# Kernel optimization log

Measured on AMD Instinct MI355X. Metric: run time of the kernel, lower is better.

## Reference

```python
import jax, jax.numpy as jnp
import numpy as np

B, T = 16, 512
S = T - 16  # sequence length after three 5x5 VALID convs and pool (H: T-4-4-4-5+1)
H = 64      # GRU hidden size


def setup_inputs() -> dict:
    key = jax.random.key(0)
    ks = jax.random.split(key, 20)
    def prm(k, shape, s=0.02):
        return jax.random.normal(k, shape, dtype=jnp.float32) * s
    return {
        "evaluation": jax.random.normal(ks[0], (B, 128, T), dtype=jnp.float32),
        "template":   jax.random.normal(ks[1], (B, 128, T), dtype=jnp.float32),
        "conv1_w": prm(ks[2], (16, 1, 5, 5), 0.05),  "conv1_b": prm(ks[3], (16,)),
        "conv2_w": prm(ks[4], (32, 16, 5, 5), 0.05), "conv2_b": prm(ks[5], (32,)),
        "conv3_w": prm(ks[6], (64, 32, 5, 5), 0.05), "conv3_b": prm(ks[7], (64,)),
        "lin1_w": prm(ks[8], (64, 3712)), "lin1_b": prm(ks[9], (64,)),
        "W_ih": prm(ks[10], (192, 64), 0.1), "W_hh": prm(ks[11], (192, 64), 0.1),
        "b_ih": prm(ks[12], (192,)),          "b_hh": prm(ks[13], (192,)),
        "att_w": prm(ks[14], (1, 64)),  "att_b": prm(ks[15], (1,)),
        "lin3_w": prm(ks[16], (128, 64)), "lin3_b": prm(ks[17], (128,)),
        "cls_w": prm(ks[18], (2, 128)),   "cls_b": prm(ks[19], (2,)),
    }


def _conv(x, w, b):
    # x: (N, C, H, W), w: (O, C, kh, kw), VALID, stride 1
    y = jax.lax.conv_general_dilated(x, w, (1, 1), 'VALID',
                                     dimension_numbers=('NCHW', 'OIHW', 'NCHW'))
    return y + b[None, :, None, None]


def _gru_seq(x, W_ih, W_hh, b_ih, b_hh):
    # x: (L, 64). One hidden state carried over the whole length (this mirrors
    # the torch module threading h0/h1 across samples in its Python loop).
    gi = x @ W_ih.T + b_ih  # (L, 192) input gates precomputed
    def step(h, gi_t):
        gh = W_hh @ h + b_hh
        r = jax.nn.sigmoid(gi_t[:H] + gh[:H])
        z = jax.nn.sigmoid(gi_t[H:2 * H] + gh[H:2 * H])
        n = jnp.tanh(gi_t[2 * H:] + r * gh[2 * H:])
        h_new = (1.0 - z) * n + z * h
        return h_new, h_new
    _, hs = jax.lax.scan(step, jnp.zeros((H,), x.dtype), gi)
    return hs  # (L, 64)


def reference(evaluation, template, conv1_w, conv1_b, conv2_w, conv2_b,
              conv3_w, conv3_b, lin1_w, lin1_b, W_ih, W_hh, b_ih, b_hh,
              att_w, att_b, lin3_w, lin3_b, cls_w, cls_b):
    # Shared conv trunk on stacked eval+template batch
    x = jnp.concatenate([evaluation, template], axis=0)      # (2B, 128, T)
    x = jnp.transpose(x, (0, 2, 1))[:, None]                 # (2B, 1, T, 128)
    x = _conv(x, conv1_w, conv1_b)                           # (2B, 16, T-4, 124)
    x = _conv(x, conv2_w, conv2_b)                           # (2B, 32, T-8, 120)
    x = _conv(x, conv3_w, conv3_b)                           # (2B, 64, T-12, 116)
    x = jax.lax.reduce_window(x, -jnp.inf, jax.lax.max,
                              (1, 1, 5, 2), (1, 1, 1, 2), 'VALID')  # (2B, 64, S, 58)
    # torch does a raw per-sample reshape (64, S, 58) -> (S, 3712)
    x = x.reshape(2 * B, S, 3712)
    x = x @ lin1_w.T + lin1_b                                # (2B, S, 64)
    # GRU: hidden carried across the batch -> one long scan per branch
    E = _gru_seq(x[:B].reshape(B * S, H), W_ih, W_hh, b_ih, b_hh).reshape(B, S, H)
    Tm = _gru_seq(x[B:].reshape(B * S, H), W_ih, W_hh, b_ih, b_hh).reshape(B, S, H)
    # alignment_weights[m, n] = <E[m], Tm[n]>, softmax over m (dim=0 per sample)
    A = jax.nn.softmax(jnp.einsum('bmd,bnd->bmn', E, Tm), axis=1)
    Tp = jnp.einsum('bmn,bnd->bmd', A, Tm)                   # template_prim
    dist = jnp.abs(Tp - E)                                    # (B, S, 64)
    att = jax.nn.softmax(jnp.einsum('bsd,d->bs', E, att_w[0]) + att_b[0], axis=1)
    rep = jnp.einsum('bs,bsd->bd', att, dist)                 # (B, 64)
    h = jax.nn.relu(rep)
    h = jax.nn.relu(h @ lin3_w.T + lin3_b)
    return h @ cls_w.T + cls_b                                # (B, 2)
```

## Files before the change

### kernel.cpp

```cpp
#include <hip/hip_runtime.h>
#include <hip/hip_bf16.h>
#include <math.h>


#define DEVI static __device__ __forceinline__
typedef __attribute__((ext_vector_type(8))) short short8;
typedef __attribute__((ext_vector_type(4))) float f32x4;
typedef __attribute__((ext_vector_type(8))) float f32x8;
typedef unsigned short ushort_t;

DEVI float fsig(float x)   { return 1.f / (1.f + __expf(-x)); }
DEVI float ftanh_(float x) { return 2.f / (1.f + __expf(-2.f * x)) - 1.f; }
DEVI float bf2f(ushort_t u) { union { unsigned int i; float f; } v; v.i = ((unsigned int)u) << 16; return v.f; }
DEVI ushort_t f2bf(float f) {
    union { float f; unsigned int i; } v; v.f = f;
    unsigned int r = v.i + 0x7FFF + ((v.i >> 16) & 1);
    return (ushort_t)(r >> 16);
}
DEVI f32x8 bf2f8(short8 s) {
    f32x8 r;
#pragma unroll
    for (int k = 0; k < 8; k++) r[k] = bf2f((ushort_t)s[k]);
    return r;
}
DEVI f32x8 max8(f32x8 a, f32x8 b) {
    f32x8 r;
#pragma unroll
    for (int k = 0; k < 8; k++) r[k] = fmaxf(a[k], b[k]);
    return r;
}

DEVI void glds16(const ushort_t* g, ushort_t* l)
{
    __builtin_amdgcn_global_load_lds(
        (const __attribute__((address_space(1))) void*)g,
        (__attribute__((address_space(3))) void*)l, 16, 0, 0);
}

__global__ void pack_w2(const float* __restrict__ w2, ushort_t* __restrict__ w2p)
{
    for (int idx = blockIdx.x * 256 + threadIdx.x; idx < 15360; idx += gridDim.x * 256) {
        int kh = idx / 3072, rem = idx % 3072;
        int kw = rem / 512;
        int co = (rem >> 4) & 31, ci = rem & 15;
        float v = (kw < 5) ? w2[((co * 16 + ci) * 5 + kh) * 5 + kw] : 0.f;
        w2p[idx] = f2bf(v);
    }
}
__global__ void pack_w3(const float* __restrict__ w3, ushort_t* __restrict__ w3p)
{
    for (int idx = blockIdx.x * 256 + threadIdx.x; idx < 51200; idx += gridDim.x * 256) {
        int kh = idx / 10240, rem = idx % 10240;
        int kw = rem / 2048;
        int co = (rem >> 5) & 63, ci = rem & 31;
        w3p[idx] = f2bf(w3[((co * 32 + ci) * 5 + kh) * 5 + kw]);
    }
}
__global__ void pack_l1w(const float* __restrict__ l1w, ushort_t* __restrict__ l1wp)
{
    for (int idx = blockIdx.x * 256 + threadIdx.x; idx < 262144; idx += gridDim.x * 256) {
        int n = idx >> 12, kp = idx & 4095;
        int r = kp >> 6, j = kp & 63;
        float v = (j < 58) ? l1w[n * 3712 + r * 58 + j] : 0.f;
        l1wp[idx] = f2bf(v);
    }
}

__global__ void conv1_kernel(const float* __restrict__ ev,
                             const float* __restrict__ tmpl,
                             const float* __restrict__ wgt,
                             const float* __restrict__ bias,
                             ushort_t* __restrict__ out, int n0)
{
    const int h0  = blockIdx.x * 4;
    const int w0  = blockIdx.y * 62;
    const int nl  = blockIdx.z;
    const int n   = n0 + nl;
    const int tid = threadIdx.x;
    const int wl  = tid & 63;
    const int cg  = tid >> 6;
    const float* src = (n < 16) ? (ev + (size_t)n * 65536)
                                : (tmpl + (size_t)(n - 16) * 65536);

    __shared__ float tin[8 * 68];
    __shared__ float tw[16 * 25];

    float acc[4][4];
#pragma unroll
    for (int j = 0; j < 4; j++)
#pragma unroll
        for (int hh = 0; hh < 4; hh++) acc[j][hh] = 0.f;

    for (int idx = tid; idx < 528; idx += 256) {
        int cc = idx >> 3, r = idx & 7;
        tin[r * 68 + cc] = src[(w0 + cc) * 512 + h0 + r];
    }
    for (int idx = tid; idx < 400; idx += 256) tw[idx] = wgt[idx];
    __syncthreads();
#pragma unroll
    for (int kh = 0; kh < 5; kh++) {
#pragma unroll
        for (int kw = 0; kw < 5; kw++) {
            float iv[4];
#pragma unroll
            for (int hh = 0; hh < 4; hh++)
                iv[hh] = tin[(hh + kh) * 68 + wl + kw];
#pragma unroll
            for (int j = 0; j < 4; j++) {
                float wv = tw[(cg * 4 + j) * 25 + kh * 5 + kw];
#pragma unroll
                for (int hh = 0; hh < 4; hh++)
                    acc[j][hh] = fmaf(wv, iv[hh], acc[j][hh]);
            }
        }
    }
    if (wl < 62) {
#pragma unroll
        for (int hh = 0; hh < 4; hh++) {
            ushort_t pk[4];
#pragma unroll
            for (int j = 0; j < 4; j++)
                pk[j] = f2bf(acc[j][hh] + bias[cg * 4 + j]);
            ushort_t* dst = out + ((size_t)(nl * 508 + h0 + hh) * 124 + w0 + wl) * 16 + cg * 4;
            *(uint2*)dst = *(uint2*)pk;
        }
    }
}

template<int CI, int CO, int NF, int MF, int NHI, int W_T, int KSTEPS,
         int KW_TOT, int H_IN, int W_IN, bool PAD2, bool HPOOL, int MAXB>
__global__ __launch_bounds__(256, MAXB) void conv_mfma(
    const ushort_t* __restrict__ in, const ushort_t* __restrict__ wpk,
    const float* __restrict__ bias, ushort_t* __restrict__ out)
{
    constexpr int H_OUT = H_IN - 4;
    constexpr int W_OUT = W_IN - 4;
    constexpr int HALO  = W_T + 6;
    constexpr int OCT   = CI / 8;
    constexpr int AROWS = 4 * NHI + 4;
    constexpr int APL   = AROWS * HALO;
    constexpr int BPL   = KW_TOT * CO;

    const int h0 = blockIdx.x * (4 * NHI);
    const int w0 = blockIdx.y * W_T;
    const int nl = blockIdx.z;
    const int tid  = threadIdx.x;
    const int wv   = tid >> 6;
    const int lane = tid & 63;
    const int l16  = lane & 15;
    const int kq   = lane >> 4;

    __shared__ __align__(16) ushort_t As[OCT * APL * 8];
    __shared__ __align__(16) ushort_t Bs[OCT * BPL * 8];

    f32x4 acc[NHI][MF][NF];
#pragma unroll
    for (int hi = 0; hi < NHI; hi++)
#pragma unroll
        for (int mi = 0; mi < MF; mi++)
#pragma unroll
            for (int ni = 0; ni < NF; ni++)
                acc[hi][mi][ni] = f32x4{0.f, 0.f, 0.f, 0.f};

    for (int idx = tid; idx < OCT * APL; idx += 256) {
        int oct = idx / APL, e = idx - oct * APL;
        int r = e / HALO, c = e - r * HALO;
        glds16(in + ((size_t)((nl * H_IN + h0 + r) * W_IN + w0 + c)) * CI + oct * 8,
               &As[idx * 8]);
    }

    const int aoct = PAD2 ? (kq & 1) : kq;
    const int kwq  = PAD2 ? (kq >> 1) : 0;

#pragma unroll
    for (int kh = 0; kh < 5; kh++) {
        __syncthreads();
        for (int idx = tid; idx < OCT * BPL; idx += 256) {
            int oct = idx / BPL, e = idx - oct * BPL;
            int kw = e / CO, co = e - kw * CO;
            glds16(wpk + ((size_t)((kh * KW_TOT + kw) * CO + co)) * CI + oct * 8,
                   &Bs[idx * 8]);
        }
        __syncthreads();
#pragma unroll
        for (int st = 0; st < KSTEPS; st++) {
            const int colq = (PAD2 ? st * 2 : st) + kwq;
            short8 bfv[NF];
#pragma unroll
            for (int ni = 0; ni < NF; ni++)
                bfv[ni] = *(const short8*)&Bs[(aoct * BPL + colq * CO + ni * 16 + l16) * 8];
#pragma unroll
            for (int hi = 0; hi < NHI; hi++) {
                short8 af[MF];
#pragma unroll
                for (int mi = 0; mi < MF; mi++)
                    af[mi] = *(const short8*)&As[(aoct * APL + (hi * 4 + wv + kh) * HALO + mi * 16 + l16 + colq) * 8];
#pragma unroll
                for (int mi = 0; mi < MF; mi++)
#pragma unroll
                    for (int ni = 0; ni < NF; ni++)
                        acc[hi][mi][ni] = __builtin_amdgcn_mfma_f32_16x16x32_bf16(
                            af[mi], bfv[ni], acc[hi][mi][ni], 0, 0, 0);
            }
        }
    }

#pragma unroll
    for (int hi = 0; hi < NHI; hi++) {
        const int h = h0 + hi * 4 + wv;
        if (h < H_OUT) {
#pragma unroll
            for (int mi = 0; mi < MF; mi++) {
#pragma unroll
                for (int ni = 0; ni < NF; ni++) {
                    int co = ni * 16 + l16;
                    float bv = bias[co];
                    if constexpr (HPOOL) {
                        const int jw = (w0 + mi * 16 + kq * 4) >> 1;
                        if (jw < 58)
                            out[((size_t)(nl * H_OUT + h) * 58 + jw) * CO + co] =
                                f2bf(fmaxf(acc[hi][mi][ni][0], acc[hi][mi][ni][1]) + bv);
                        if (jw + 1 < 58)
                            out[((size_t)(nl * H_OUT + h) * 58 + jw + 1) * CO + co] =
                                f2bf(fmaxf(acc[hi][mi][ni][2], acc[hi][mi][ni][3]) + bv);
                    } else {
#pragma unroll
                        for (int reg = 0; reg < 4; reg++) {
                            int w = w0 + mi * 16 + kq * 4 + reg;
                            if (w < W_OUT)
                                out[((size_t)(nl * H_OUT + h) * W_OUT + w) * CO + co] =
                                    f2bf(acc[hi][mi][ni][reg] + bv);
                        }
                    }
                }
            }
        }
    }
}

__global__ __launch_bounds__(512) void pool_fused(const ushort_t* __restrict__ a3h,
                                                  ushort_t* __restrict__ pooled)
{
    const int nl = blockIdx.y;
    const int s0 = blockIdx.x * 16;
    const int t  = threadIdx.x;
    __shared__ ushort_t L[4 * 3712];

    const int j = t >> 3, oct = t & 7;
    const ushort_t* base = a3h + (size_t)nl * 1856000 + (size_t)j * 64 + oct * 8;
    ushort_t* dst = pooled + (size_t)nl * 1841152;

#define LOADROW(rr) bf2f8(*(const short8*)(base + (size_t)(rr) * 3712))
    f32x8 w0, w1, w2v, w3v;
    if (t < 464) {
        w0  = LOADROW(s0);
        w1  = LOADROW(s0 + 1);
        w2v = LOADROW(s0 + 2);
        w3v = LOADROW(s0 + 3);
    }
    for (int g = 0; g < 4; g++) {
        if (t < 464) {
#pragma unroll
            for (int k = 0; k < 4; k++) {
                int s = s0 + g * 4 + k;
                f32x8 w4 = LOADROW(s + 4);
                f32x8 mx = max8(max8(max8(w0, w1), max8(w2v, w3v)), w4);
#pragma unroll
                for (int u = 0; u < 8; u++)
                    L[k * 3712 + (oct * 8 + u) * 58 + j] = f2bf(mx[u]);
                w0 = w1; w1 = w2v; w2v = w3v; w3v = w4;
            }
        }
        __syncthreads();
        const int sg = s0 + g * 4;
        for (int e = t; e < 14848; e += 512) {
            int k = e / 3712, r = e - k * 3712;
            int c = r / 58, jj = r - c * 58;
            dst[(size_t)c * 28768 + (sg + k) * 58 + jj] = L[e];
        }
        __syncthreads();
    }
#undef LOADROW
}

__global__ __launch_bounds__(256) void lin1_mfma(
    const ushort_t* __restrict__ pooled, const ushort_t* __restrict__ l1wp,
    float* __restrict__ xb, int n0, int RT)
{
    const int mt  = blockIdx.x;
    const int kqb = blockIdx.y;
    const int r0  = mt * 64;
    const int t   = threadIdx.x;
    const int wv  = t >> 6, lane = t & 63, l16 = lane & 15, kq = lane >> 4;

    __shared__ __align__(16) ushort_t As[8 * 64 * 8];
    __shared__ __align__(16) ushort_t Bs[8 * 64 * 8];

    f32x4 acc[4];
#pragma unroll
    for (int ni = 0; ni < 4; ni++) acc[ni] = f32x4{0.f, 0.f, 0.f, 0.f};

    for (int kb = 0; kb < 16; kb++) {
        const int k0 = kqb * 1024 + kb * 64;
        const int r  = k0 >> 6;
        __syncthreads();
        for (int idx = t; idx < 512; idx += 256) {
            int oct = idx >> 6, row = idx & 63;
            int rr = r0 + row;
            short8 v = short8{0, 0, 0, 0, 0, 0, 0, 0};
            if (rr < RT)
                v = *(const short8*)(pooled + (size_t)rr * 3712 + r * 58 + oct * 8);
            *(short8*)&As[idx * 8] = v;
        }
        for (int idx = t; idx < 512; idx += 256) {
            int oct = idx >> 6, co = idx & 63;
            *(short8*)&Bs[idx * 8] =
                *(const short8*)(l1wp + (size_t)co * 4096 + k0 + oct * 8);
        }
        __syncthreads();
#pragma unroll
        for (int st = 0; st < 2; st++) {
            short8 af = *(const short8*)&As[((st * 4 + kq) * 64 + wv * 16 + l16) * 8];
#pragma unroll
            for (int ni = 0; ni < 4; ni++) {
                short8 bfv = *(const short8*)&Bs[((st * 4 + kq) * 64 + ni * 16 + l16) * 8];
                acc[ni] = __builtin_amdgcn_mfma_f32_16x16x32_bf16(af, bfv, acc[ni], 0, 0, 0);
            }
        }
    }
#pragma unroll
    for (int ni = 0; ni < 4; ni++) {
        int co = ni * 16 + l16;
#pragma unroll
        for (int reg = 0; reg < 4; reg++) {
            int rr = r0 + wv * 16 + kq * 4 + reg;
            if (rr < RT)
                atomicAdd(&xb[((size_t)n0 * 496 + rr) * 64 + co], acc[ni][reg]);
        }
    }
}

__global__ __launch_bounds__(192) void gi_kernel(
    const float* __restrict__ x, const float* __restrict__ Wih,
    const float* __restrict__ bih, const float* __restrict__ l1b,
    float* __restrict__ gi)
{
    const int r0 = blockIdx.x * 64;
    const int j  = threadIdx.x;
    __shared__ float wls[192 * 65];
    __shared__ float xl[64 * 64];

    for (int idx = j; idx < 12288; idx += 192)
        wls[(idx >> 6) * 65 + (idx & 63)] = Wih[idx];
    for (int idx = j; idx < 4096; idx += 192)
        xl[idx] = x[(size_t)r0 * 64 + idx] + l1b[idx & 63];
    __syncthreads();

    float w[64];
#pragma unroll
    for (int d = 0; d < 64; d++) w[d] = wls[j * 65 + d];
    const float bj = bih[j];

    for (int s = 0; s < 64; s++) {
        float a = bj;
#pragma unroll
        for (int d = 0; d < 64; d++) a = fmaf(w[d], xl[s * 64 + d], a);
        gi[(size_t)(r0 + s) * 192 + j] = a;
    }
}

__global__ __launch_bounds__(192, 3) void gru_kernel(
    const float* __restrict__ gi, const float* __restrict__ Whh,
    const float* __restrict__ bhh, float* __restrict__ Eo,
    float* __restrict__ To)
{
    const int c  = blockIdx.x;
    const int br = (c >= 496) ? 1 : 0;
    const int q  = c - br * 496;
    const int j  = threadIdx.x;
    const float* gb = gi + (size_t)br * 7936 * 192;
    float* out = br ? To : Eo;

    float w[64];
#pragma unroll
    for (int k = 0; k < 64; k++) w[k] = Whh[j * 64 + k];
    const float bh = bhh[j];

    __shared__ __align__(16) float hs[64];
    __shared__ float gs[192];
    __shared__ float gnl[64];

    float h[64];
#pragma unroll
    for (int k = 0; k < 64; k++) h[k] = 0.f;
    float hown = 0.f;

    const int cs  = q * 16;
    int start = cs - 96;
    if (start < 0) start = 0;
    const int end = cs + 16;

    const bool isN  = (j >= 128);
    const bool isW0 = (j < 64);

    float pg[4];
#pragma unroll
    for (int u = 0; u < 4; u++) {
        int s = start + u;
        pg[u] = (s < end) ? gb[(size_t)s * 192 + j] : 0.f;
    }

    int s = start;
    while (s < end) {
#pragma unroll
        for (int u = 0; u < 4; u++) {
            if (s < end) {
                float g = pg[u];
                int sp = s + 4;
                if (sp < end) pg[u] = gb[(size_t)sp * 192 + j];
                float a0 = bh, a1 = 0.f;
#pragma unroll
                for (int k = 0; k < 64; k += 2) {
                    a0 = fmaf(w[k],     h[k],     a0);
                    a1 = fmaf(w[k + 1], h[k + 1], a1);
                }
                float gh = a0 + a1;
                gs[j] = isN ? gh : (gh + g);
                if (isN) gnl[j - 128] = g;
                __syncthreads();
                float hn = 0.f;
                if (isW0) {
                    float r  = fsig(gs[j]);
                    float z  = fsig(gs[64 + j]);
                    float nv = ftanh_(gnl[j] + r * gs[128 + j]);
                    hn = (1.f - z) * nv + z * hown;
                    hown = hn;
                    hs[j] = hn;
                }
                __syncthreads();
#pragma unroll
                for (int k = 0; k < 16; k++) {
                    float4 v = ((const float4*)hs)[k];
                    h[4 * k + 0] = v.x; h[4 * k + 1] = v.y;
                    h[4 * k + 2] = v.z; h[4 * k + 3] = v.w;
                }
                if (isW0 && s >= cs) out[(size_t)s * 64 + j] = hn;
                s++;
            }
        }
    }
}

__global__ void scores_kernel(const float* __restrict__ E,
                              const float* __restrict__ Tm,
                              float* __restrict__ S,
                              float* __restrict__ zsum)
{
    const int b  = blockIdx.z;
    const int m0 = blockIdx.y * 32;
    const int n0 = blockIdx.x * 64;
    const int t  = threadIdx.x;
    const int nl = t & 63, mg = t >> 6;
    __shared__ float El[32 * 64];
    __shared__ float Tms[64 * 65];

    for (int idx = t; idx < 2048; idx += 256) {
        int r = idx >> 6, d = idx & 63;
        int m = m0 + r;
        El[idx] = (m < 496) ? E[((size_t)b * 496 + m) * 64 + d] : 0.f;
    }
    for (int idx = t; idx < 4096; idx += 256) {
        int r = idx >> 6, d = idx & 63;
        int n = n0 + r;
        Tms[d * 65 + r] = (n < 496) ? Tm[((size_t)b * 496 + n) * 64 + d] : 0.f;
    }
    __syncthreads();

    float acc[8];
#pragma unroll
    for (int j = 0; j < 8; j++) acc[j] = 0.f;
#pragma unroll 4
    for (int d = 0; d < 64; d++) {
        float tv = Tms[d * 65 + nl];
#pragma unroll
        for (int j = 0; j < 8; j++)
            acc[j] = fmaf(El[(mg * 8 + j) * 64 + d], tv, acc[j]);
    }
    int n = n0 + nl;
    if (n < 496) {
        float lsum = 0.f;
#pragma unroll
        for (int j = 0; j < 8; j++) {
            int m = m0 + mg * 8 + j;
            if (m < 496) {
                S[((size_t)b * 496 + m) * 496 + n] = acc[j];
                lsum += __expf(acc[j]);
            }
        }
        atomicAdd(&zsum[b * 496 + n], lsum);
    }
}

__global__ void tp_kernel(const float* __restrict__ S,
                          const float* __restrict__ Tm,
                          const float* __restrict__ zsum,
                          float* __restrict__ Tp)
{
    const int b  = blockIdx.y;
    const int m0 = blockIdx.x * 32;
    const int t  = threadIdx.x;
    const int d  = t & 63, mg = t >> 6;
    __shared__ float As2[32 * 128];
    __shared__ float Ts[128 * 64];
    float acc[8];
#pragma unroll
    for (int j = 0; j < 8; j++) acc[j] = 0.f;

    for (int nc = 0; nc < 512; nc += 128) {
        __syncthreads();
        for (int idx = t; idx < 4096; idx += 256) {
            int r = idx >> 7, cc = idx & 127;
            int m = m0 + r, n = nc + cc;
            As2[idx] = (m < 496 && n < 496)
                          ? __expf(S[((size_t)b * 496 + m) * 496 + n]) : 0.f;
        }
        for (int idx = t; idx < 8192; idx += 256) {
            int r = idx >> 6, dd = idx & 63;
            int n = nc + r;
            Ts[idx] = (n < 496)
                          ? Tm[((size_t)b * 496 + n) * 64 + dd] / zsum[b * 496 + n]
                          : 0.f;
        }
        __syncthreads();
#pragma unroll 4
        for (int nn = 0; nn < 128; nn++) {
            float tv = Ts[nn * 64 + d];
#pragma unroll
            for (int j = 0; j < 8; j++)
                acc[j] = fmaf(As2[(mg * 8 + j) * 128 + nn], tv, acc[j]);
        }
    }
#pragma unroll
    for (int j = 0; j < 8; j++) {
        int m = m0 + mg * 8 + j;
        if (m < 496) Tp[((size_t)b * 496 + m) * 64 + d] = acc[j];
    }
}

__global__ void attrep_kernel(const float* __restrict__ E,
                              const float* __restrict__ Tp,
                              const float* __restrict__ attw,
                              const float* __restrict__ attb,
                              float* __restrict__ rep)
{
    const int b = blockIdx.x;
    const int t = threadIdx.x;
    __shared__ float aw[64];
    __shared__ float lg[496];
    __shared__ float att[496];
    __shared__ float redm[4], reds[4];
    __shared__ float part[256];

    if (t < 64) aw[t] = attw[t];
    __syncthreads();
    for (int s = t; s < 496; s += 256) {
        const float* Er = E + ((size_t)b * 496 + s) * 64;
        float a = 0.f;
#pragma unroll
        for (int dd = 0; dd < 64; dd++) a = fmaf(Er[dd], aw[dd], a);
        lg[s] = a + attb[0];
    }
    __syncthreads();
    float m = -1e30f;
    for (int s = t; s < 496; s += 256) m = fmaxf(m, lg[s]);
    for (int off = 32; off > 0; off >>= 1)
        m = fmaxf(m, __shfl_xor(m, off, 64));
    if ((t & 63) == 0) redm[t >> 6] = m;
    __syncthreads();
    m = fmaxf(fmaxf(redm[0], redm[1]), fmaxf(redm[2], redm[3]));
    float sum = 0.f;
    for (int s = t; s < 496; s += 256) {
        float e = __expf(lg[s] - m);
        att[s] = e;
        sum += e;
    }
    for (int off = 32; off > 0; off >>= 1) sum += __shfl_xor(sum, off, 64);
    if ((t & 63) == 0) reds[t >> 6] = sum;
    __syncthreads();
    float inv = 1.f / (reds[0] + reds[1] + reds[2] + reds[3]);

    const int d = t & 63, sg = t >> 6;
    float p = 0.f;
    for (int k = 0; k < 124; k++) {
        int s = sg + 4 * k;
        size_t o = ((size_t)b * 496 + s) * 64 + d;
        p = fmaf(att[s] * inv, fabsf(Tp[o] - E[o]), p);
    }
    part[t] = p;
    __syncthreads();
    if (t < 64)
        rep[b * 64 + t] = part[t] + part[64 + t] + part[128 + t] + part[192 + t];
}

__global__ void mlp_kernel(const float* __restrict__ rep,
                           const float* __restrict__ W3,
                           const float* __restrict__ b3,
                           const float* __restrict__ Wc,
                           const float* __restrict__ bc,
                           float* __restrict__ out)
{
    const int b = blockIdx.x;
    const int t = threadIdx.x;
    __shared__ float hr[64];
    __shared__ float h2[128];
    if (t < 64) hr[t] = fmaxf(rep[b * 64 + t], 0.f);
    __syncthreads();
    float a = b3[t];
#pragma unroll
    for (int d = 0; d < 64; d++) a = fmaf(W3[t * 64 + d], hr[d], a);
    h2[t] = fmaxf(a, 0.f);
    __syncthreads();
    if (t < 2) {
        float o = bc[t];
        for (int k = 0; k < 128; k++) o = fmaf(Wc[t * 128 + k], h2[k], o);
        out[b * 2 + t] = o;
    }
}

extern "C" void kernel_launch(void* const* d_in, const int* in_sizes, int n_in,
                              void* d_out, int out_size, void* d_ws,
                              size_t ws_size, hipStream_t stream)
{
    const float* ev   = (const float*)d_in[0];
    const float* tmpl = (const float*)d_in[1];
    const float* w1   = (const float*)d_in[2];
    const float* b1   = (const float*)d_in[3];
    const float* w2   = (const float*)d_in[4];
    const float* b2   = (const float*)d_in[5];
    const float* w3   = (const float*)d_in[6];
    const float* b3   = (const float*)d_in[7];
    const float* l1w  = (const float*)d_in[8];
    const float* l1b  = (const float*)d_in[9];
    const float* wih  = (const float*)d_in[10];
    const float* whh  = (const float*)d_in[11];
    const float* bih  = (const float*)d_in[12];
    const float* bhh  = (const float*)d_in[13];
    const float* attw = (const float*)d_in[14];
    const float* attb = (const float*)d_in[15];
    const float* l3w  = (const float*)d_in[16];
    const float* l3b  = (const float*)d_in[17];
    const float* clw  = (const float*)d_in[18];
    const float* clb  = (const float*)d_in[19];

    float* ws = (float*)d_ws;
    float* xb    = ws;
    float* Eb    = xb + 1015808ull;
    float* Tb    = Eb + 507904ull;
    float* Tpb   = Tb + 507904ull;
    float* repb  = Tpb + 507904ull;
    float* w2pf  = repb + 1024ull;
    float* w3pf  = w2pf + 7680ull;
    float* l1wpf = w3pf + 25600ull;
    float* zsumb = l1wpf + 131072ull;
    float* arena = zsumb + 8192ull;
    const size_t PERSIST = 2713088ull;

    ushort_t* w2p  = (ushort_t*)w2pf;
    ushort_t* w3p  = (ushort_t*)w3pf;
    ushort_t* l1wp = (ushort_t*)l1wpf;

    const int cand[6] = {32, 16, 8, 4, 2, 1};
    int C = 0;
    for (int ci = 0; ci < 6; ci++) {
        size_t a = (size_t)cand[ci] * 2823680ull + 16384ull;
        if (a < 3936256ull) a = 3936256ull;
        if ((PERSIST + a) * sizeof(float) <= ws_size) { C = cand[ci]; break; }
    }
    if (C == 0) return;

    float*    S1 = arena;
    float*    S2 = arena + (size_t)C * 967680ull + 8192ull;
    float*    gib = arena;
    float*    Sb  = arena;

    ushort_t* a2  = (ushort_t*)S1;
    ushort_t* pooled = (ushort_t*)S1;
    ushort_t* a1  = (ushort_t*)S2;
    ushort_t* a3h = (ushort_t*)S2;

    hipMemsetAsync(xb, 0, 1015808ull * sizeof(float), stream);
    hipMemsetAsync(zsumb, 0, 8192ull * sizeof(float), stream);
    pack_w2<<<15, 256, 0, stream>>>(w2, w2p);
    pack_w3<<<50, 256, 0, stream>>>(w3, w3p);
    pack_l1w<<<256, 256, 0, stream>>>(l1w, l1wp);

    const int RT = C * 496;
    const int mtiles = (RT + 63) / 64;

    for (int n0 = 0; n0 < 32; n0 += C) {
        conv1_kernel<<<dim3(127, 2, C), 256, 0, stream>>>(ev, tmpl, w1, b1, a1, n0);
        conv_mfma<16, 32, 2, 4, 2, 64, 3, 6, 508, 124, true, false, 4>
            <<<dim3(63, 2, C), 256, 0, stream>>>(a1, w2p, b2, a2);
        conv_mfma<32, 64, 4, 2, 2, 32, 5, 5, 504, 120, false, true, 3>
            <<<dim3(63, 4, C), 256, 0, stream>>>(a2, w3p, b3, a3h);
        pool_fused<<<dim3(31, C), 512, 0, stream>>>(a3h, pooled);
        lin1_mfma<<<dim3(mtiles, 4), 256, 0, stream>>>(pooled, l1wp, xb, n0, RT);
    }

    gi_kernel<<<248, 192, 0, stream>>>(xb, wih, bih, l1b, gib);
    gru_kernel<<<992, 192, 0, stream>>>(gib, whh, bhh, Eb, Tb);

    scores_kernel<<<dim3(8, 16, 16), 256, 0, stream>>>(Eb, Tb, Sb, zsumb);
    tp_kernel<<<dim3(16, 16), 256, 0, stream>>>(Sb, Tb, zsumb, Tpb);

    attrep_kernel<<<16, 256, 0, stream>>>(Eb, Tpb, attw, attb, repb);
    mlp_kernel<<<16, 128, 0, stream>>>(repb, l3w, l3b, clw, clb,
                                       (float*)d_out);
}
```

Before: 779.1 us.

## Merge weight-pack kernels, precompute conv B-tile addresses, async-load lin1 weights

Folds the three weight-packing kernels and the zsum memset into a single launch to cut launch overhead. In the MFMA conv kernel, the per-kh weight-tile source and destination addresses are computed once before the kh loop, removing integer divides from the inner loop. The lin1 kernel's weight tile now goes straight from global memory to LDS with global_load_lds instead of staging through registers. Each piece is small, and together they trim fixed overhead and address arithmetic but add register pressure for the stored pointers.

```diff
diff --git a/kernel.cpp b/kernel.cpp
--- a/kernel.cpp
+++ b/kernel.cpp
@@ -37,33 +37,33 @@
         (__attribute__((address_space(3))) void*)l, 16, 0, 0);
 }
 
-__global__ void pack_w2(const float* __restrict__ w2, ushort_t* __restrict__ w2p)
-{
-    for (int idx = blockIdx.x * 256 + threadIdx.x; idx < 15360; idx += gridDim.x * 256) {
+__global__ void pack_all(const float* __restrict__ w2, const float* __restrict__ w3,
+                         const float* __restrict__ l1w,
+                         ushort_t* __restrict__ w2p, ushort_t* __restrict__ w3p,
+                         ushort_t* __restrict__ l1wp, float* __restrict__ zsum)
+{
+    const int gid = blockIdx.x * 256 + threadIdx.x;
+    const int gsz = gridDim.x * 256;
+    for (int idx = gid; idx < 15360; idx += gsz) {
         int kh = idx / 3072, rem = idx % 3072;
         int kw = rem / 512;
         int co = (rem >> 4) & 31, ci = rem & 15;
         float v = (kw < 5) ? w2[((co * 16 + ci) * 5 + kh) * 5 + kw] : 0.f;
         w2p[idx] = f2bf(v);
     }
-}
-__global__ void pack_w3(const float* __restrict__ w3, ushort_t* __restrict__ w3p)
-{
-    for (int idx = blockIdx.x * 256 + threadIdx.x; idx < 51200; idx += gridDim.x * 256) {
+    for (int idx = gid; idx < 51200; idx += gsz) {
         int kh = idx / 10240, rem = idx % 10240;
         int kw = rem / 2048;
         int co = (rem >> 5) & 63, ci = rem & 31;
         w3p[idx] = f2bf(w3[((co * 32 + ci) * 5 + kh) * 5 + kw]);
     }
-}
-__global__ void pack_l1w(const float* __restrict__ l1w, ushort_t* __restrict__ l1wp)
-{
-    for (int idx = blockIdx.x * 256 + threadIdx.x; idx < 262144; idx += gridDim.x * 256) {
+    for (int idx = gid; idx < 262144; idx += gsz) {
         int n = idx >> 12, kp = idx & 4095;
         int r = kp >> 6, j = kp & 63;
         float v = (j < 58) ? l1w[n * 3712 + r * 58 + j] : 0.f;
         l1wp[idx] = f2bf(v);
     }
+    for (int idx = gid; idx < 8192; idx += gsz) zsum[idx] = 0.f;
 }
 
 __global__ void conv1_kernel(const float* __restrict__ ev,
@@ -140,6 +140,9 @@
     constexpr int AROWS = 4 * NHI + 4;
     constexpr int APL   = AROWS * HALO;
     constexpr int BPL   = KW_TOT * CO;
+    constexpr int BTOT  = OCT * BPL;
+    constexpr int BSTG  = (BTOT + 255) / 256;
+    constexpr int KHOFF = KW_TOT * CO * CI;
 
     const int h0 = blockIdx.x * (4 * NHI);
     const int w0 = blockIdx.y * W_T;
@@ -151,7 +154,7 @@
     const int kq   = lane >> 4;
 
     __shared__ __align__(16) ushort_t As[OCT * APL * 8];
-    __shared__ __align__(16) ushort_t Bs[OCT * BPL * 8];
+    __shared__ __align__(16) ushort_t Bs[BTOT * 8];
 
     f32x4 acc[NHI][MF][NF];
 #pragma unroll
@@ -169,18 +172,28 @@
                &As[idx * 8]);
     }
 
+    const ushort_t* bsrc[BSTG];
+    ushort_t*       bdst[BSTG];
+#pragma unroll
+    for (int sb = 0; sb < BSTG; sb++) {
+        int idx = tid + sb * 256;
+        if (idx < BTOT) {
+            int oct = idx / BPL, e = idx - oct * BPL;
+            int kw = e / CO, co = e - kw * CO;
+            bsrc[sb] = wpk + ((size_t)(kw * CO + co)) * CI + oct * 8;
+            bdst[sb] = &Bs[idx * 8];
+        } else { bsrc[sb] = nullptr; bdst[sb] = nullptr; }
+    }
+
     const int aoct = PAD2 ? (kq & 1) : kq;
     const int kwq  = PAD2 ? (kq >> 1) : 0;
 
 #pragma unroll
     for (int kh = 0; kh < 5; kh++) {
         __syncthreads();
-        for (int idx = tid; idx < OCT * BPL; idx += 256) {
-            int oct = idx / BPL, e = idx - oct * BPL;
-            int kw = e / CO, co = e - kw * CO;
-            glds16(wpk + ((size_t)((kh * KW_TOT + kw) * CO + co)) * CI + oct * 8,
-                   &Bs[idx * 8]);
-        }
+#pragma unroll
+        for (int sb = 0; sb < BSTG; sb++)
+            if (bsrc[sb]) glds16(bsrc[sb] + kh * KHOFF, bdst[sb]);
         __syncthreads();
 #pragma unroll
         for (int st = 0; st < KSTEPS; st++) {
@@ -312,11 +325,9 @@
                 v = *(const short8*)(pooled + (size_t)rr * 3712 + r * 58 + oct * 8);
             *(short8*)&As[idx * 8] = v;
         }
-        for (int idx = t; idx < 512; idx += 256) {
-            int oct = idx >> 6, co = idx & 63;
-            *(short8*)&Bs[idx * 8] =
-                *(const short8*)(l1wp + (size_t)co * 4096 + k0 + oct * 8);
-        }
+        for (int idx = t; idx < 512; idx += 256)
+            glds16(l1wp + (size_t)(idx & 63) * 4096 + k0 + (idx >> 6) * 8,
+                   &Bs[idx * 8]);
         __syncthreads();
 #pragma unroll
         for (int st = 0; st < 2; st++) {
@@ -689,10 +700,7 @@
     ushort_t* a3h = (ushort_t*)S2;
 
     hipMemsetAsync(xb, 0, 1015808ull * sizeof(float), stream);
-    hipMemsetAsync(zsumb, 0, 8192ull * sizeof(float), stream);
-    pack_w2<<<15, 256, 0, stream>>>(w2, w2p);
-    pack_w3<<<50, 256, 0, stream>>>(w3, w3p);
-    pack_l1w<<<256, 256, 0, stream>>>(l1w, l1wp);
+    pack_all<<<256, 256, 0, stream>>>(w2, w3, l1w, w2p, w3p, l1wp, zsumb);
 
     const int RT = C * 496;
     const int mtiles = (RT + 63) / 64;
```

Measured after the change: 770.1 us. No clear change (-1.2%).
